# Optimization experiments

Hardware: AMD Instinct MI355X
Metric: run time of the kernel (lower is better)

The kernel has to match this reference:

```python
import jax, jax.numpy as jnp
import numpy as np

NUM_HEADS = 16
D_MODEL = 1024
BATCH = 8
SEQ = 1024


def setup_inputs() -> dict:
    key = jax.random.key(0)
    ks = jax.random.split(key, 8)
    inv = 1.0 / np.sqrt(D_MODEL)
    return {
        "query": jax.random.normal(ks[0], (BATCH, SEQ, D_MODEL), dtype=jnp.float32),
        "key": jax.random.normal(ks[1], (BATCH, SEQ, D_MODEL), dtype=jnp.float32),
        "value": jax.random.normal(ks[2], (BATCH, SEQ, D_MODEL), dtype=jnp.float32),
        "mask": jax.random.randint(ks[3], (BATCH, SEQ), 0, 2, dtype=jnp.int32),
        "Wq": jax.random.normal(ks[4], (D_MODEL, D_MODEL), dtype=jnp.float32) * inv,
        "bq": jax.random.normal(ks[5], (D_MODEL,), dtype=jnp.float32) * inv,
        "Wo": jax.random.normal(ks[6], (D_MODEL, D_MODEL), dtype=jnp.float32) * inv,
        "bo": jax.random.normal(ks[7], (D_MODEL,), dtype=jnp.float32) * inv,
    }


def reference(query, key, value, mask, Wq, bq, Wo, bo):
    b, s, d = query.shape
    H = NUM_HEADS
    dk = d // H
    # NOTE: the original torch module (faithfully reproduced) applies
    # query_project to query, key AND value; key/value projections are dead.
    def proj(x):
        return (x @ Wq.T + bq).reshape(b, s, H, dk).transpose(0, 2, 1, 3)  # (b,H,s,dk)

    q, k, v = proj(query), proj(key), proj(value)

    m = mask.astype(query.dtype)                       # (b,s)
    score_mask = (m[:, :, None] * m[:, None, :])[:, None]  # (b,1,s,s), broadcasts over heads

    scale = 1.0 / jnp.sqrt(jnp.asarray(dk, dtype=query.dtype))
    score = jnp.einsum("bhqd,bhkd->bhqk", q, k) * scale  # (b,H,s,s)
    score = jnp.where(score_mask == 0, jnp.asarray(-1e9, dtype=score.dtype), score)
    # softmax then post-softmax mask multiply (the non-standard double-masking)
    p_attn = jax.nn.softmax(score, axis=-1) * score_mask  # (b,H,s,s)

    x = jnp.einsum("bhqk,bhkd->bhqd", p_attn, v)  # (b,H,s,dk)
    x = x.transpose(0, 2, 1, 3).reshape(b, s, d)
    out = x @ Wo.T + bo
    return out, p_attn
```

## Files before the change

kernel.cpp:

```cpp
#include <hip/hip_runtime.h>
#include <cstddef>
#include <cstdint>

#define BATCH   8
#define SEQ     1024
#define DMODEL  1024
#define NHEADS  16
#define DKH     64
#define NE      (BATCH*SEQ*DMODEL)
#define WE      (DMODEL*DMODEL)
#define WE4     (WE/4)

typedef __attribute__((ext_vector_type(8))) short bf16x8;
typedef __attribute__((ext_vector_type(4))) short s16x4;
typedef __attribute__((ext_vector_type(4))) float f32x4;

#define MFMA16(a,b,c) __builtin_amdgcn_mfma_f32_16x16x32_bf16(a,b,c,0,0,0)

__device__ __forceinline__ unsigned short f2bf(float f) {
    uint32_t u = __float_as_uint(f);
    u += 0x7fffu + ((u >> 16) & 1u);
    return (unsigned short)(u >> 16);
}
__device__ __forceinline__ float bf2f(unsigned short s) {
    return __uint_as_float(((uint32_t)s) << 16);
}

__device__ __forceinline__ void gload16(const void* g, void* l) {
    __builtin_amdgcn_global_load_lds(
        (const __attribute__((address_space(1))) void*)g,
        (__attribute__((address_space(3))) void*)l, 16, 0, 0);
}

__global__ void cvt_w(const float* __restrict__ wq, const float* __restrict__ wo,
                      unsigned short* __restrict__ wqh, unsigned short* __restrict__ woh)
{
    const int i = blockIdx.x * blockDim.x + threadIdx.x;
    const float* src; unsigned short* dst; int j;
    if (i < WE4) { src = wq; dst = wqh; j = i; }
    else         { src = wo; dst = woh; j = i - WE4; }
    const f32x4 x = ((const f32x4*)src)[j];
    s16x4 h4;
    #pragma unroll
    for (int e = 0; e < 4; ++e) h4[e] = (short)f2bf(x[e]);
    ((s16x4*)dst)[j] = h4;
}

#define GBM 128
#define GBN 128
#define GBK 32

template<int OUTMODE>
__global__ __launch_bounds__(256, 2)
void gemm_mfma(const float* __restrict__ Aq, const float* __restrict__ Ak,
               const float* __restrict__ Av, const unsigned short* __restrict__ Ab,
               const unsigned short* __restrict__ Whi, const float* __restrict__ bias,
               unsigned short* __restrict__ Ohi, unsigned short* __restrict__ Ovt,
               float* __restrict__ Of)
{
    __shared__ unsigned short sA[2][GBM * GBK];
    __shared__ unsigned short sW[2][GBM * GBK];

    const int tid = threadIdx.x, lane = tid & 63, wid = tid >> 6;
    const int cpx = gridDim.x >> 3;
    const int L = (blockIdx.x & 7) * cpx + (blockIdx.x >> 3);
    const int n0 = (L & 7) * GBN, m0 = (L >> 3) * GBM;
    const int wm = (wid >> 1) * 64, wn = (wid & 1) * 64;
    const int lo = lane & 15, hi4 = lane >> 4;

    const int gs = (lane & 3) ^ ((lane >> 3) & 3);
    const size_t wrow0 = (size_t)(n0 + wid * 32 + (lane >> 2));
    const unsigned short* wSrc0 = &Whi[wrow0 * DMODEL + gs * 8];
    const unsigned short* wSrc1 = &Whi[(wrow0 + 16) * DMODEL + gs * 8];

    const int seg = (OUTMODE == 3) ? (m0 >> 13) : 0;
    const float* Af = (OUTMODE == 3)
        ? (seg == 0 ? Aq : (seg == 1 ? Ak : Av)) : nullptr;
    const int mloc = m0 & 8191;
    const int arow_s = (tid * 2) >> 2;
    const int aslot0 = (tid * 2) & 3;
    const int akey = (arow_s >> 1) & 3;
    const float* aF0 = (OUTMODE == 3) ? &Af[(size_t)(mloc + arow_s) * DMODEL + (aslot0 ^ akey) * 8] : nullptr;
    const float* aF1 = (OUTMODE == 3) ? &Af[(size_t)(mloc + arow_s) * DMODEL + ((aslot0 + 1) ^ akey) * 8] : nullptr;
    const size_t arow0 = (size_t)(m0 + wid * 32 + (lane >> 2));
    const unsigned short* aSrc0 = (OUTMODE == 2) ? &Ab[arow0 * DMODEL + gs * 8] : nullptr;
    const unsigned short* aSrc1 = (OUTMODE == 2) ? &Ab[(arow0 + 16) * DMODEL + gs * 8] : nullptr;

    f32x4 acc[4][4] = {};
    f32x4 ar0, ar1, ar2, ar3;

    if (OUTMODE == 3) {
        ar0 = *(const f32x4*)aF0; ar1 = *(const f32x4*)(aF0 + 4);
        ar2 = *(const f32x4*)aF1; ar3 = *(const f32x4*)(aF1 + 4);
        bf16x8 h0, h1;
        #pragma unroll
        for (int e = 0; e < 4; ++e) {
            h0[e] = (short)f2bf(ar0[e]); h0[4 + e] = (short)f2bf(ar1[e]);
            h1[e] = (short)f2bf(ar2[e]); h1[4 + e] = (short)f2bf(ar3[e]);
        }
        *(bf16x8*)&sA[0][arow_s * GBK + aslot0 * 8]       = h0;
        *(bf16x8*)&sA[0][arow_s * GBK + (aslot0 + 1) * 8] = h1;
    } else {
        unsigned short* dA = &sA[0][(wid * 2) * 512];
        gload16(aSrc0, dA);  gload16(aSrc1, dA + 512);
    }
    {
        unsigned short* dW = &sW[0][(wid * 2) * 512];
        gload16(wSrc0, dW);  gload16(wSrc1, dW + 512);
    }

    for (int kt = 0; kt < DMODEL / GBK; ++kt) {
        __syncthreads();
        const int nb = (kt + 1) & 1;
        if (kt + 1 < DMODEL / GBK) {
            const int kn = (kt + 1) * GBK;
            if (OUTMODE == 3) {
                ar0 = *(const f32x4*)(aF0 + kn); ar1 = *(const f32x4*)(aF0 + kn + 4);
                ar2 = *(const f32x4*)(aF1 + kn); ar3 = *(const f32x4*)(aF1 + kn + 4);
            } else {
                unsigned short* dA = &sA[nb][(wid * 2) * 512];
                gload16(aSrc0 + kn, dA);  gload16(aSrc1 + kn, dA + 512);
            }
            unsigned short* dW = &sW[nb][(wid * 2) * 512];
            gload16(wSrc0 + kn, dW);  gload16(wSrc1 + kn, dW + 512);
        }
        const unsigned short* aB = &sA[kt & 1][0];
        const unsigned short* wB = &sW[kt & 1][0];
        const int swz = (hi4 ^ ((lo >> 1) & 3)) * 8;
        bf16x8 ah[4], bh_[4];
        #pragma unroll
        for (int m = 0; m < 4; ++m)
            ah[m] = *(const bf16x8*)&aB[(wm + m * 16 + lo) * GBK + swz];
        #pragma unroll
        for (int n = 0; n < 4; ++n)
            bh_[n] = *(const bf16x8*)&wB[(wn + n * 16 + lo) * GBK + swz];
        #pragma unroll
        for (int m = 0; m < 4; ++m)
            #pragma unroll
            for (int n = 0; n < 4; ++n)
                acc[m][n] = MFMA16(ah[m], bh_[n], acc[m][n]);

        if (OUTMODE == 3 && kt + 1 < DMODEL / GBK) {
            bf16x8 h0, h1;
            #pragma unroll
            for (int e = 0; e < 4; ++e) {
                h0[e] = (short)f2bf(ar0[e]); h0[4 + e] = (short)f2bf(ar1[e]);
                h1[e] = (short)f2bf(ar2[e]); h1[4 + e] = (short)f2bf(ar3[e]);
            }
            *(bf16x8*)&sA[nb][arow_s * GBK + aslot0 * 8]       = h0;
            *(bf16x8*)&sA[nb][arow_s * GBK + (aslot0 + 1) * 8] = h1;
        }
    }

    #pragma unroll
    for (int n = 0; n < 4; ++n) {
        const int col = n0 + wn + n * 16 + lo;
        const float bv = bias[col];
        #pragma unroll
        for (int m = 0; m < 4; ++m) {
            if (OUTMODE == 3 && seg == 2) {
                const int row0 = (m0 + wm + m * 16 + hi4 * 4) & 8191;
                const int b = row0 >> 10, s0_ = row0 & 1023;
                const int h = col >> 6, di = col & 63;
                s16x4 o;
                #pragma unroll
                for (int j = 0; j < 4; ++j) o[j] = (short)f2bf(acc[m][n][j] + bv);
                *(s16x4*)&Ovt[(((size_t)(b * NHEADS + h)) * DKH + di) * SEQ + s0_] = o;
            } else {
                #pragma unroll
                for (int j = 0; j < 4; ++j) {
                    const int row = m0 + wm + m * 16 + hi4 * 4 + j;
                    const float f = acc[m][n][j] + bv;
                    if (OUTMODE == 3) {
                        const int rs = row & 8191;
                        const int b = rs >> 10, s = rs & 1023;
                        const int h = col >> 6, di = col & 63;
                        unsigned short* dst = Ohi + (size_t)seg * NE;
                        dst[(((size_t)(b * NHEADS + h)) * SEQ + s) * DKH + di] = f2bf(f);
                    } else {
                        Of[(size_t)row * DMODEL + col] = f;
                    }
                }
            }
        }
    }
}

#define ALD 72

__global__ __launch_bounds__(512, 4)
void attn_fused(const unsigned short* __restrict__ qhi, const unsigned short* __restrict__ khi,
                const unsigned short* __restrict__ vt, const int* __restrict__ mask,
                float* __restrict__ pattn, unsigned short* __restrict__ xb)
{
    __shared__ unsigned short sQh[128 * ALD];
    __shared__ unsigned short sKh[64 * ALD];
    __shared__ unsigned short sVt[64 * ALD];
    __shared__ int sM[SEQ];
    __shared__ float sP32[8][16 * 68];

    const int blk = blockIdx.x;
    const int idx = blk >> 3;
    const int bh = (blk & 7) * 16 + (idx & 15);
    const int qt = idx >> 4;
    const int b = bh >> 4, h = bh & 15;
    const int q0 = qt * 128;
    const int tid = threadIdx.x, lane = tid & 63, wid = tid >> 6;
    const int lo = lane & 15, hi = lane >> 4;

    *(int2*)&sM[tid * 2] = *(const int2*)&mask[b * SEQ + tid * 2];
    #pragma unroll
    for (int c = 0; c < 2; ++c) {
        const int id = tid * 2 + c, row = id >> 3, col = (id & 7) * 8;
        *(bf16x8*)&sQh[row * ALD + col] =
            *(const bf16x8*)&qhi[((size_t)bh * SEQ + q0 + row) * DKH + col];
    }
    __syncthreads();

    const int qrow = wid * 16 + lo;
    bf16x8 aqh[2];
    aqh[0] = *(const bf16x8*)&sQh[qrow * ALD + hi * 8];
    aqh[1] = *(const bf16x8*)&sQh[qrow * ALD + 32 + hi * 8];
    int mqr[4];
    #pragma unroll
    for (int j = 0; j < 4; ++j) mqr[j] = sM[q0 + wid * 16 + hi * 4 + j];

    const int srow = tid >> 3, scol = (tid & 7) * 8;
    const unsigned short* kbase = &khi[(size_t)bh * SEQ * DKH + (size_t)srow * DKH + scol];
    const unsigned short* vbase = &vt[(size_t)bh * DKH * SEQ + (size_t)srow * SEQ + scol];

    float l4[4] = {0.f, 0.f, 0.f, 0.f};
    bf16x8 kr = *(const bf16x8*)kbase;
    for (int kt = 0; kt < 16; ++kt) {
        __syncthreads();
        *(bf16x8*)&sKh[srow * ALD + scol] = kr;
        __syncthreads();
        if (kt < 15) kr = *(const bf16x8*)(kbase + (size_t)(kt + 1) * 64 * DKH);
        f32x4 acc4[4] = {};
        #pragma unroll
        for (int ks = 0; ks < 2; ++ks)
            #pragma unroll
            for (int n = 0; n < 4; ++n)
                acc4[n] = MFMA16(aqh[ks],
                    *(const bf16x8*)&sKh[(n * 16 + lo) * ALD + ks * 32 + hi * 8], acc4[n]);
        #pragma unroll
        for (int n = 0; n < 4; ++n) {
            const int mkc = sM[kt * 64 + n * 16 + lo];
            #pragma unroll
            for (int j = 0; j < 4; ++j)
                l4[j] += (mqr[j] && mkc) ? __expf(acc4[n][j] * 0.125f) : 0.f;
        }
    }
    float rinv[4];
    #pragma unroll
    for (int j = 0; j < 4; ++j) {
        float s = l4[j];
        #pragma unroll
        for (int o = 1; o < 16; o <<= 1) s += __shfl_xor(s, o, 16);
        rinv[j] = (s > 0.f) ? (1.0f / s) : 0.f;
    }

    f32x4 oacc[4] = {};
    kr = *(const bf16x8*)kbase;
    bf16x8 vr = *(const bf16x8*)vbase;
    for (int kt = 0; kt < 16; ++kt) {
        __syncthreads();
        *(bf16x8*)&sKh[srow * ALD + scol] = kr;
        *(bf16x8*)&sVt[srow * ALD + scol] = vr;
        __syncthreads();
        if (kt < 15) {
            kr = *(const bf16x8*)(kbase + (size_t)(kt + 1) * 64 * DKH);
            vr = *(const bf16x8*)(vbase + (kt + 1) * 64);
        }
        f32x4 acc4[4] = {};
        #pragma unroll
        for (int ks = 0; ks < 2; ++ks)
            #pragma unroll
            for (int n = 0; n < 4; ++n)
                acc4[n] = MFMA16(aqh[ks],
                    *(const bf16x8*)&sKh[(n * 16 + lo) * ALD + ks * 32 + hi * 8], acc4[n]);

        #pragma unroll
        for (int n = 0; n < 4; ++n) {
            const int mkc = sM[kt * 64 + n * 16 + lo];
            #pragma unroll
            for (int j = 0; j < 4; ++j) {
                const float p = (mqr[j] && mkc) ? __expf(acc4[n][j] * 0.125f) * rinv[j] : 0.f;
                sP32[wid][(hi * 4 + j) * 68 + n * 16 + lo] = p;
            }
        }
        asm volatile("s_waitcnt lgkmcnt(0)" ::: "memory");
        __builtin_amdgcn_sched_barrier(0);

        #pragma unroll
        for (int rr = 0; rr < 4; ++rr) {
            const int prow = rr * 4 + hi;
            const f32x4 pv = *(const f32x4*)&sP32[wid][prow * 68 + lo * 4];
            __builtin_nontemporal_store(pv,
                (f32x4*)&pattn[((size_t)bh * SEQ + q0 + wid * 16 + prow) * SEQ + kt * 64 + lo * 4]);
        }
        #pragma unroll
        for (int ks = 0; ks < 2; ++ks) {
            const float* pp = &sP32[wid][lo * 68 + ks * 32 + hi * 8];
            const f32x4 p0 = *(const f32x4*)pp;
            const f32x4 p1 = *(const f32x4*)(pp + 4);
            bf16x8 ap;
            #pragma unroll
            for (int e = 0; e < 4; ++e) { ap[e] = (short)f2bf(p0[e]); ap[4 + e] = (short)f2bf(p1[e]); }
            #pragma unroll
            for (int n = 0; n < 4; ++n)
                oacc[n] = MFMA16(ap,
                    *(const bf16x8*)&sVt[(n * 16 + lo) * ALD + ks * 32 + hi * 8], oacc[n]);
        }
    }

    #pragma unroll
    for (int n = 0; n < 4; ++n)
        #pragma unroll
        for (int j = 0; j < 4; ++j) {
            const int row = q0 + wid * 16 + hi * 4 + j;
            const int col = h * DKH + n * 16 + lo;
            xb[(size_t)(b * SEQ + row) * DMODEL + col] = f2bf(oacc[n][j]);
        }
}

extern "C" void kernel_launch(void* const* d_in, const int* in_sizes, int n_in,
                              void* d_out, int out_size, void* d_ws, size_t ws_size,
                              hipStream_t stream) {
    (void)in_sizes; (void)n_in; (void)out_size; (void)ws_size;

    const float* query = (const float*)d_in[0];
    const float* key   = (const float*)d_in[1];
    const float* value = (const float*)d_in[2];
    const int*   mask  = (const int*)d_in[3];
    const float* Wq    = (const float*)d_in[4];
    const float* bq    = (const float*)d_in[5];
    const float* Wo    = (const float*)d_in[6];
    const float* bo    = (const float*)d_in[7];

    float* out   = (float*)d_out;
    float* pattn = out + (size_t)NE;

    char* w = (char*)d_ws;
    unsigned short* wqhi = (unsigned short*)w;  w += (size_t)WE * 2;
    unsigned short* wohi = (unsigned short*)w;  w += (size_t)WE * 2;
    unsigned short* qhi  = (unsigned short*)w;  w += (size_t)NE * 2;
    unsigned short* khi  = (unsigned short*)w;  w += (size_t)NE * 2;
    unsigned short* vt   = (unsigned short*)w;  w += (size_t)NE * 2;
    unsigned short* xb   = (unsigned short*)w;  w += (size_t)NE * 2;

    cvt_w<<<2 * WE4 / 256, 256, 0, stream>>>(Wq, Wo, wqhi, wohi);

    gemm_mfma<3><<<8 * (3 * BATCH * SEQ) / GBM, 256, 0, stream>>>(
        query, key, value, nullptr, wqhi, bq, qhi, vt, nullptr);

    attn_fused<<<BATCH * NHEADS * (SEQ / 128), 512, 0, stream>>>(qhi, khi, vt, mask, pattn, xb);

    gemm_mfma<2><<<8 * (BATCH * SEQ) / GBM, 256, 0, stream>>>(
        nullptr, nullptr, nullptr, xb, wohi, bo, nullptr, nullptr, out);
}
```

Before: 264.0 us.

## Double-buffer K/V tiles via direct global-to-LDS loads with XOR swizzle

The attention kernel now streams K and V tiles straight from global memory into double-buffered, XOR-swizzled LDS using gload16, instead of staging them through registers. This cuts one barrier per iteration and lets the next tile's load overlap the current tile's MFMAs. LDS is repacked into one aliased buffer, with the Q staging area reused for the probability scratch, to make room for the second buffers. The projection's fp32 output store also becomes nontemporal. Correctness depends on gload16 completing before the barrier that precedes each buffer's use.

```diff
diff --git a/kernel.cpp b/kernel.cpp
--- a/kernel.cpp
+++ b/kernel.cpp
@@ -178,7 +178,7 @@
                         unsigned short* dst = Ohi + (size_t)seg * NE;
                         dst[(((size_t)(b * NHEADS + h)) * SEQ + s) * DKH + di] = f2bf(f);
                     } else {
-                        Of[(size_t)row * DMODEL + col] = f;
+                        __builtin_nontemporal_store(f, &Of[(size_t)row * DMODEL + col]);
                     }
                 }
             }
@@ -187,17 +187,19 @@
 }
 
 #define ALD 72
+#define KTE 4096
 
 __global__ __launch_bounds__(512, 4)
 void attn_fused(const unsigned short* __restrict__ qhi, const unsigned short* __restrict__ khi,
                 const unsigned short* __restrict__ vt, const int* __restrict__ mask,
                 float* __restrict__ pattn, unsigned short* __restrict__ xb)
 {
-    __shared__ unsigned short sQh[128 * ALD];
-    __shared__ unsigned short sKh[64 * ALD];
-    __shared__ unsigned short sVt[64 * ALD];
-    __shared__ int sM[SEQ];
-    __shared__ float sP32[8][16 * 68];
+    __shared__ __align__(16) char smem[71680];
+    unsigned short* sQh = (unsigned short*)smem;
+    float*          sP32 = (float*)smem;
+    unsigned short* sKh = (unsigned short*)(smem + 34816);
+    unsigned short* sVt = (unsigned short*)(smem + 51200);
+    int*            sM  = (int*)(smem + 67584);
 
     const int blk = blockIdx.x;
     const int idx = blk >> 3;
@@ -208,6 +210,11 @@
     const int tid = threadIdx.x, lane = tid & 63, wid = tid >> 6;
     const int lo = lane & 15, hi = lane >> 4;
 
+    const int sr8 = tid >> 3;
+    const int sw  = (tid & 7) ^ (sr8 & 7);
+    const unsigned short* kSrc = &khi[(size_t)bh * SEQ * DKH + (size_t)sr8 * DKH + sw * 8];
+    const unsigned short* vSrc = &vt[(size_t)bh * DKH * SEQ + (size_t)sr8 * SEQ + sw * 8];
+
     *(int2*)&sM[tid * 2] = *(const int2*)&mask[b * SEQ + tid * 2];
     #pragma unroll
     for (int c = 0; c < 2; ++c) {
@@ -215,6 +222,7 @@
         *(bf16x8*)&sQh[row * ALD + col] =
             *(const bf16x8*)&qhi[((size_t)bh * SEQ + q0 + row) * DKH + col];
     }
+    gload16(kSrc, &sKh[0] + wid * 512);
     __syncthreads();
 
     const int qrow = wid * 16 + lo;
@@ -225,24 +233,20 @@
     #pragma unroll
     for (int j = 0; j < 4; ++j) mqr[j] = sM[q0 + wid * 16 + hi * 4 + j];
 
-    const int srow = tid >> 3, scol = (tid & 7) * 8;
-    const unsigned short* kbase = &khi[(size_t)bh * SEQ * DKH + (size_t)srow * DKH + scol];
-    const unsigned short* vbase = &vt[(size_t)bh * DKH * SEQ + (size_t)srow * SEQ + scol];
-
     float l4[4] = {0.f, 0.f, 0.f, 0.f};
-    bf16x8 kr = *(const bf16x8*)kbase;
     for (int kt = 0; kt < 16; ++kt) {
-        __syncthreads();
-        *(bf16x8*)&sKh[srow * ALD + scol] = kr;
-        __syncthreads();
-        if (kt < 15) kr = *(const bf16x8*)(kbase + (size_t)(kt + 1) * 64 * DKH);
+        if (kt < 15)
+            gload16(kSrc + (size_t)(kt + 1) * 64 * DKH, &sKh[((kt + 1) & 1) * KTE] + wid * 512);
+        const unsigned short* kB = &sKh[(kt & 1) * KTE];
         f32x4 acc4[4] = {};
         #pragma unroll
         for (int ks = 0; ks < 2; ++ks)
             #pragma unroll
-            for (int n = 0; n < 4; ++n)
+            for (int n = 0; n < 4; ++n) {
+                const int row = n * 16 + lo;
                 acc4[n] = MFMA16(aqh[ks],
-                    *(const bf16x8*)&sKh[(n * 16 + lo) * ALD + ks * 32 + hi * 8], acc4[n]);
+                    *(const bf16x8*)&kB[row * 64 + (((ks << 2) + hi) ^ (row & 7)) * 8], acc4[n]);
+            }
         #pragma unroll
         for (int n = 0; n < 4; ++n) {
             const int mkc = sM[kt * 64 + n * 16 + lo];
@@ -250,6 +254,7 @@
             for (int j = 0; j < 4; ++j)
                 l4[j] += (mqr[j] && mkc) ? __expf(acc4[n][j] * 0.125f) : 0.f;
         }
+        __syncthreads();
     }
     float rinv[4];
     #pragma unroll
@@ -261,24 +266,26 @@
     }
 
     f32x4 oacc[4] = {};
-    kr = *(const bf16x8*)kbase;
-    bf16x8 vr = *(const bf16x8*)vbase;
+    gload16(kSrc, &sKh[0] + wid * 512);
+    gload16(vSrc, &sVt[0] + wid * 512);
+    __syncthreads();
     for (int kt = 0; kt < 16; ++kt) {
-        __syncthreads();
-        *(bf16x8*)&sKh[srow * ALD + scol] = kr;
-        *(bf16x8*)&sVt[srow * ALD + scol] = vr;
-        __syncthreads();
         if (kt < 15) {
-            kr = *(const bf16x8*)(kbase + (size_t)(kt + 1) * 64 * DKH);
-            vr = *(const bf16x8*)(vbase + (kt + 1) * 64);
-        }
+            const int nb = ((kt + 1) & 1);
+            gload16(kSrc + (size_t)(kt + 1) * 64 * DKH, &sKh[nb * KTE] + wid * 512);
+            gload16(vSrc + (kt + 1) * 64,               &sVt[nb * KTE] + wid * 512);
+        }
+        const unsigned short* kB = &sKh[(kt & 1) * KTE];
+        const unsigned short* vB = &sVt[(kt & 1) * KTE];
         f32x4 acc4[4] = {};
         #pragma unroll
         for (int ks = 0; ks < 2; ++ks)
             #pragma unroll
-            for (int n = 0; n < 4; ++n)
+            for (int n = 0; n < 4; ++n) {
+                const int row = n * 16 + lo;
                 acc4[n] = MFMA16(aqh[ks],
-                    *(const bf16x8*)&sKh[(n * 16 + lo) * ALD + ks * 32 + hi * 8], acc4[n]);
+                    *(const bf16x8*)&kB[row * 64 + (((ks << 2) + hi) ^ (row & 7)) * 8], acc4[n]);
+            }
 
         #pragma unroll
         for (int n = 0; n < 4; ++n) {
@@ -286,7 +293,7 @@
             #pragma unroll
             for (int j = 0; j < 4; ++j) {
                 const float p = (mqr[j] && mkc) ? __expf(acc4[n][j] * 0.125f) * rinv[j] : 0.f;
-                sP32[wid][(hi * 4 + j) * 68 + n * 16 + lo] = p;
+                sP32[wid * (16 * 68) + (hi * 4 + j) * 68 + n * 16 + lo] = p;
             }
         }
         asm volatile("s_waitcnt lgkmcnt(0)" ::: "memory");
@@ -295,23 +302,26 @@
         #pragma unroll
         for (int rr = 0; rr < 4; ++rr) {
             const int prow = rr * 4 + hi;
-            const f32x4 pv = *(const f32x4*)&sP32[wid][prow * 68 + lo * 4];
+            const f32x4 pv = *(const f32x4*)&sP32[wid * (16 * 68) + prow * 68 + lo * 4];
             __builtin_nontemporal_store(pv,
                 (f32x4*)&pattn[((size_t)bh * SEQ + q0 + wid * 16 + prow) * SEQ + kt * 64 + lo * 4]);
         }
         #pragma unroll
         for (int ks = 0; ks < 2; ++ks) {
-            const float* pp = &sP32[wid][lo * 68 + ks * 32 + hi * 8];
+            const float* pp = &sP32[wid * (16 * 68) + lo * 68 + ks * 32 + hi * 8];
             const f32x4 p0 = *(const f32x4*)pp;
             const f32x4 p1 = *(const f32x4*)(pp + 4);
             bf16x8 ap;
             #pragma unroll
             for (int e = 0; e < 4; ++e) { ap[e] = (short)f2bf(p0[e]); ap[4 + e] = (short)f2bf(p1[e]); }
             #pragma unroll
-            for (int n = 0; n < 4; ++n)
+            for (int n = 0; n < 4; ++n) {
+                const int row = n * 16 + lo;
                 oacc[n] = MFMA16(ap,
-                    *(const bf16x8*)&sVt[(n * 16 + lo) * ALD + ks * 32 + hi * 8], oacc[n]);
-        }
+                    *(const bf16x8*)&vB[row * 64 + (((ks << 2) + hi) ^ (row & 7)) * 8], oacc[n]);
+            }
+        }
+        __syncthreads();
     }
 
     #pragma unroll
```

Result: no change. 259.8 us, median of 2 (-1.6%).
